# Kernel tuning notes

Hardware: AMD Instinct MI355X
Metric: run time of the kernel (lower is better)

## Reference

```python
import jax, jax.numpy as jnp
import numpy as np

T, D, E, K = 8192, 4096, 64, 8


def setup_inputs() -> dict:
    key = jax.random.key(0)
    k1, k2, k3, k4 = jax.random.split(key, 4)
    x = jax.random.normal(k1, (T, D), dtype=jnp.float32)
    # nn.Linear stores weight as [out_features, in_features]
    Wg = jax.random.normal(k2, (E, D), dtype=jnp.float32) * (1.0 / np.sqrt(D))
    Wc = jax.random.normal(k3, (E, D), dtype=jnp.float32) * (1.0 / np.sqrt(D))
    extra_scale = jnp.zeros((E,), dtype=jnp.float32)  # init zeros as in module
    extra_bias = jax.random.normal(k4, (E,), dtype=jnp.float32) * 0.01
    return {"x": x, "Wg": Wg, "Wc": Wc, "extra_scale": extra_scale,
            "extra_bias": extra_bias, "topk": K}


def reference(x, Wg, Wc, extra_scale, extra_bias, topk):
    # scores = |classifier(x) * silu(gate(x))|, softmax in fp32
    gate = jnp.einsum('td,ed->te', x, Wg)        # [T, E]
    cls = jnp.einsum('td,ed->te', x, Wc)         # [T, E]
    scores = jnp.abs(cls * jax.nn.silu(gate))
    scores = jax.nn.softmax(scores.astype(jnp.float32), axis=-1)
    biased = scores + extra_bias[None, :]        # load-balance bias, used only for selection
    _, indices = jax.lax.top_k(biased, topk)     # [T, K]
    original = 1.0 + scores * extra_scale[None, :]
    weights = jnp.take_along_axis(original, indices, axis=1)  # [T, K]
    return weights.astype(x.dtype), indices
```

## Files before the change

kernel.cpp:

```cpp
#include <hip/hip_runtime.h>
#include <math.h>


#define T_DIM 8192
#define D_DIM 4096
#define E_DIM 64
#define N2    128
#define KTOP  8
#define MB_ROWS 64

#define LDS_H2S 512
#define LDS_PS  1040
#define LDS_RGS (3 * LDS_PS)
#define LDS_BFS (2 * LDS_RGS)

typedef __attribute__((ext_vector_type(8)))  short bfrag8;
typedef __attribute__((ext_vector_type(16))) float f32x16;
typedef __attribute__((ext_vector_type(4)))  float f4;

__device__ __forceinline__ unsigned short f2bf_rne(float f) {
    unsigned int u = __float_as_uint(f);
    unsigned int r = u + 0x7fffu + ((u >> 16) & 1u);
    return (unsigned short)(r >> 16);
}
__device__ __forceinline__ float bf2f(unsigned short h) {
    return __uint_as_float(((unsigned int)h) << 16);
}
__device__ __forceinline__ void split3(float v, unsigned short& h,
                                       unsigned short& m, unsigned short& l) {
    h = f2bf_rne(v);
    const float r1 = v - bf2f(h);
    m = f2bf_rne(r1);
    const float r2 = r1 - bf2f(m);
    l = f2bf_rne(r2);
}

__global__ __launch_bounds__(256)
void router_prep(const float* __restrict__ Wg, const float* __restrict__ Wc,
                 unsigned short* __restrict__ Wpk)
{
    const int t   = blockIdx.x * 256 + threadIdx.x;
    const int col = t >> 9;
    const int ch  = t & 511;
    const int k   = ch << 3;

    const float* src = (col < E_DIM) ? (Wg + (size_t)col * D_DIM)
                                     : (Wc + (size_t)(col - E_DIM) * D_DIM);
    const float4 w0 = ((const float4*)(src + k))[0];
    const float4 w1 = ((const float4*)(src + k))[1];
    const float v[8] = {w0.x, w0.y, w0.z, w0.w, w1.x, w1.y, w1.z, w1.w};

    unsigned short hv[8], mv[8], lv[8];
    #pragma unroll
    for (int j = 0; j < 8; ++j) split3(v[j], hv[j], mv[j], lv[j]);

    const int k32 = k >> 5, h2 = (k >> 4) & 1, lh = (k >> 3) & 1;
    const int n = col >> 5, lane = lh * 32 + (col & 31);
    const size_t base = ((((size_t)k32 * 4 + n) * 3 + 0) * 2 + h2) * 512 + (size_t)lane * 8;
    *(ushort4*)(Wpk + base)          = make_ushort4(hv[0], hv[1], hv[2], hv[3]);
    *(ushort4*)(Wpk + base + 4)      = make_ushort4(hv[4], hv[5], hv[6], hv[7]);
    *(ushort4*)(Wpk + base + 1024)   = make_ushort4(mv[0], mv[1], mv[2], mv[3]);
    *(ushort4*)(Wpk + base + 1028)   = make_ushort4(mv[4], mv[5], mv[6], mv[7]);
    *(ushort4*)(Wpk + base + 2048)   = make_ushort4(lv[0], lv[1], lv[2], lv[3]);
    *(ushort4*)(Wpk + base + 2052)   = make_ushort4(lv[4], lv[5], lv[6], lv[7]);
}

__global__ __launch_bounds__(256, 4)
void router_gemm(const float* __restrict__ x,
                 const unsigned short* __restrict__ Wpk,
                 float* __restrict__ P,
                 int sliceK)
{
    __shared__ unsigned short sF[2 * LDS_BFS];

    const int tid  = threadIdx.x;
    const int lane = tid & 63;
    const int wc   = tid >> 6;
    const int l31  = lane & 31;
    const int lh   = lane >> 5;
    const int mb   = blockIdx.x;
    const int ks   = blockIdx.y;
    const int k0   = ks * sliceK;
    const int NT   = sliceK >> 5;
    const int brow0 = mb * MB_ROWS;

    const int srow = tid >> 3;
    const int kq   = tid & 7;
    const int h2w  = kq >> 2;
    const int lew  = ((kq >> 1) & 1) * 32 + srow;
    const int jw   = (kq & 1) * 4;
    const int wbase = h2w * LDS_H2S + lew * 8 + jw;
    const float* gsrc0 = x + (size_t)(brow0 + srow) * D_DIM + k0 + kq * 4;
    const float* gsrc1 = gsrc0 + (size_t)32 * D_DIM;

    f32x16 acc[2];
    #pragma unroll
    for (int rg = 0; rg < 2; ++rg)
        #pragma unroll
        for (int r = 0; r < 16; ++r) acc[rg][r] = 0.f;

    #define WRITE_HALF(v_, bf_, rg_)                                             \
        {                                                                        \
            ushort4 hv_, mv_, lv_;                                               \
            unsigned short h_, m_, l_;                                           \
            split3((v_).x, h_, m_, l_); hv_.x = h_; mv_.x = m_; lv_.x = l_;      \
            split3((v_).y, h_, m_, l_); hv_.y = h_; mv_.y = m_; lv_.y = l_;      \
            split3((v_).z, h_, m_, l_); hv_.z = h_; mv_.z = m_; lv_.z = l_;      \
            split3((v_).w, h_, m_, l_); hv_.w = h_; mv_.w = m_; lv_.w = l_;      \
            const int o_ = (bf_) * LDS_BFS + (rg_) * LDS_RGS + wbase;            \
            *(ushort4*)&sF[o_]              = hv_;                               \
            *(ushort4*)&sF[o_ + LDS_PS]     = mv_;                               \
            *(ushort4*)&sF[o_ + 2 * LDS_PS] = lv_;                               \
        }

    {
        const f4 v0 = __builtin_nontemporal_load((const f4*)gsrc0);
        const f4 v1 = __builtin_nontemporal_load((const f4*)gsrc1);
        WRITE_HALF(v0, 0, 0);
        WRITE_HALF(v1, 0, 1);
    }
    f4 xa0 = {0,0,0,0}, xa1 = {0,0,0,0};
    f4 xb0 = {0,0,0,0}, xb1 = {0,0,0,0};
    if (NT > 1) {
        xa0 = __builtin_nontemporal_load((const f4*)(gsrc0 + 32));
        xa1 = __builtin_nontemporal_load((const f4*)(gsrc1 + 32));
    }
    asm volatile("s_waitcnt lgkmcnt(0)" ::: "memory");
    __builtin_amdgcn_s_barrier();

    for (int t = 0; t < NT; ++t) {
        const int bf = t & 1;
        const int fbase = bf * LDS_BFS;

        if (t + 2 < NT) {
            xb0 = __builtin_nontemporal_load((const f4*)(gsrc0 + (t + 2) * 32));
            xb1 = __builtin_nontemporal_load((const f4*)(gsrc1 + (t + 2) * 32));
        }

        const size_t k32 = (size_t)((k0 + t * 32) >> 5);
        #pragma unroll
        for (int h2 = 0; h2 < 2; ++h2) {
            const unsigned short* bb =
                Wpk + ((((k32 * 4 + wc) * 3 + 0) * 2 + h2) * 64 + lane) * 8;
            const bfrag8 bh = *(const bfrag8*)(bb);
            const bfrag8 bm = *(const bfrag8*)(bb + 1024);
            const bfrag8 bl = *(const bfrag8*)(bb + 2048);
            #pragma unroll
            for (int rg = 0; rg < 2; ++rg) {
                const int ab = fbase + rg * LDS_RGS + h2 * LDS_H2S + lane * 8;
                const bfrag8 ah = *(const bfrag8*)&sF[ab];
                const bfrag8 am = *(const bfrag8*)&sF[ab + LDS_PS];
                const bfrag8 al = *(const bfrag8*)&sF[ab + 2 * LDS_PS];
                acc[rg] = __builtin_amdgcn_mfma_f32_32x32x16_bf16(ah, bl, acc[rg], 0, 0, 0);
                acc[rg] = __builtin_amdgcn_mfma_f32_32x32x16_bf16(al, bh, acc[rg], 0, 0, 0);
                acc[rg] = __builtin_amdgcn_mfma_f32_32x32x16_bf16(am, bm, acc[rg], 0, 0, 0);
                acc[rg] = __builtin_amdgcn_mfma_f32_32x32x16_bf16(ah, bm, acc[rg], 0, 0, 0);
                acc[rg] = __builtin_amdgcn_mfma_f32_32x32x16_bf16(am, bh, acc[rg], 0, 0, 0);
                acc[rg] = __builtin_amdgcn_mfma_f32_32x32x16_bf16(ah, bh, acc[rg], 0, 0, 0);
            }
        }

        if (t + 1 < NT) {
            WRITE_HALF(xa0, bf ^ 1, 0);
            WRITE_HALF(xa1, bf ^ 1, 1);
        }
        asm volatile("s_waitcnt lgkmcnt(0)" ::: "memory");
        __builtin_amdgcn_s_barrier();
        xa0 = xb0; xa1 = xb1;
    }
    #undef WRITE_HALF

    #pragma unroll
    for (int rg = 0; rg < 2; ++rg) {
        float* Pb = P + ((size_t)ks * T_DIM + brow0 + rg * 32) * N2 + wc * 32 + l31;
        #pragma unroll
        for (int r = 0; r < 16; ++r) {
            const int wrow = (r & 3) + 8 * (r >> 2) + 4 * lh;
            __builtin_nontemporal_store(acc[rg][r], &Pb[(size_t)wrow * N2]);
        }
    }
}

__global__ __launch_bounds__(256)
void router_topk(const float* __restrict__ P,
                 const float* __restrict__ scale,
                 const float* __restrict__ bias,
                 float* __restrict__ out,
                 int ksplit)
{
    const int lane = threadIdx.x & 63;
    const int wid  = threadIdx.x >> 6;
    const int row  = blockIdx.x * 4 + wid;

    float g = 0.f, c = 0.f;
    for (int ks = 0; ks < ksplit; ++ks) {
        const float* p = P + ((size_t)ks * T_DIM + row) * N2;
        g += p[lane];
        c += p[E_DIM + lane];
    }
    const float sg = g / (1.f + expf(-g));
    const float v  = fabsf(c * sg);

    float m = v;
    #pragma unroll
    for (int off = 32; off >= 1; off >>= 1) m = fmaxf(m, __shfl_xor(m, off));
    const float e = expf(v - m);
    float Z = e;
    #pragma unroll
    for (int off = 32; off >= 1; off >>= 1) Z += __shfl_xor(Z, off);
    const float s = e / Z;

    const float sc  = scale[lane];
    float cur = s + bias[lane];

    float myw = 0.f; int myi = 0;
    #pragma unroll
    for (int j = 0; j < KTOP; ++j) {
        float bv = cur; int bi = lane;
        #pragma unroll
        for (int off = 32; off >= 1; off >>= 1) {
            const float ov = __shfl_xor(bv, off);
            const int   oi = __shfl_xor(bi, off);
            if (ov > bv || (ov == bv && oi < bi)) { bv = ov; bi = oi; }
        }
        const float s_bi  = __shfl(s,  bi);
        const float sc_bi = __shfl(sc, bi);
        const float w = 1.f + s_bi * sc_bi;
        if (lane == j)  { myw = w; myi = bi; }
        if (lane == bi) cur = -INFINITY;
    }

    if (lane < KTOP) {
        out[(size_t)row * KTOP + lane] = myw;
        out[(size_t)T_DIM * KTOP + (size_t)row * KTOP + lane] = (float)myi;
    }
}

extern "C" void kernel_launch(void* const* d_in, const int* in_sizes, int n_in,
                              void* d_out, int out_size, void* d_ws, size_t ws_size,
                              hipStream_t stream)
{
    const float* x  = (const float*)d_in[0];
    const float* Wg = (const float*)d_in[1];
    const float* Wc = (const float*)d_in[2];
    const float* sc = (const float*)d_in[3];
    const float* bs = (const float*)d_in[4];
    float* out = (float*)d_out;
    float* P   = (float*)d_ws;

    const size_t PER = (size_t)T_DIM * N2 * sizeof(float);
    const size_t WSP = (size_t)N2 * D_DIM * sizeof(unsigned short);

    int S = 8;
    while (S > 1 && (size_t)S * PER + 3 * WSP > ws_size) S >>= 1;
    const int sliceK = D_DIM / S;

    unsigned short* Wpk = (unsigned short*)((char*)d_ws + (size_t)S * PER);

    router_prep<<<256, 256, 0, stream>>>(Wg, Wc, Wpk);
    router_gemm<<<dim3(T_DIM / MB_ROWS, S), 256, 0, stream>>>(x, Wpk, P, sliceK);
    router_topk<<<T_DIM / 4, 256, 0, stream>>>(P, sc, bs, out, S);
}
```

Measured before the change: 249.0 us.

## Process two K-tiles per barrier with four-slot LDS ring and MFMA priority

Restructures the GEMM main loop to handle two 32-wide K tiles per iteration. It uses a four-slot LDS ring, batches all weight fragment loads for both tiles up front, and prefetches x two tiles ahead. This halves the number of barriers and waitcnts per K slice and raises memory-level parallelism. It also wraps the MFMA block in s_setprio. The cost is double the LDS footprint and more registers, so occupancy is lowered from 4 to 3 blocks per CU. The loop assumes NT is even and silently drops a trailing tile otherwise.

```diff
diff --git a/kernel.cpp b/kernel.cpp
--- a/kernel.cpp
+++ b/kernel.cpp
@@ -12,7 +12,7 @@
 #define LDS_H2S 512
 #define LDS_PS  1040
 #define LDS_RGS (3 * LDS_PS)
-#define LDS_BFS (2 * LDS_RGS)
+#define LDS_TS  (2 * LDS_RGS)
 
 typedef __attribute__((ext_vector_type(8)))  short bfrag8;
 typedef __attribute__((ext_vector_type(16))) float f32x16;
@@ -65,13 +65,13 @@
     *(ushort4*)(Wpk + base + 2052)   = make_ushort4(lv[4], lv[5], lv[6], lv[7]);
 }
 
-__global__ __launch_bounds__(256, 4)
+__global__ __launch_bounds__(256, 3)
 void router_gemm(const float* __restrict__ x,
                  const unsigned short* __restrict__ Wpk,
                  float* __restrict__ P,
                  int sliceK)
 {
-    __shared__ unsigned short sF[2 * LDS_BFS];
+    __shared__ unsigned short sF[4 * LDS_TS];
 
     const int tid  = threadIdx.x;
     const int lane = tid & 63;
@@ -82,6 +82,7 @@
     const int ks   = blockIdx.y;
     const int k0   = ks * sliceK;
     const int NT   = sliceK >> 5;
+    const int NP   = NT >> 1;
     const int brow0 = mb * MB_ROWS;
 
     const int srow = tid >> 3;
@@ -99,7 +100,7 @@
         #pragma unroll
         for (int r = 0; r < 16; ++r) acc[rg][r] = 0.f;
 
-    #define WRITE_HALF(v_, bf_, rg_)                                             \
+    #define WRITE_HALF(v_, slot_, rg_)                                           \
         {                                                                        \
             ushort4 hv_, mv_, lv_;                                               \
             unsigned short h_, m_, l_;                                           \
@@ -107,68 +108,106 @@
             split3((v_).y, h_, m_, l_); hv_.y = h_; mv_.y = m_; lv_.y = l_;      \
             split3((v_).z, h_, m_, l_); hv_.z = h_; mv_.z = m_; lv_.z = l_;      \
             split3((v_).w, h_, m_, l_); hv_.w = h_; mv_.w = m_; lv_.w = l_;      \
-            const int o_ = (bf_) * LDS_BFS + (rg_) * LDS_RGS + wbase;            \
+            const int o_ = (slot_) * LDS_TS + (rg_) * LDS_RGS + wbase;           \
             *(ushort4*)&sF[o_]              = hv_;                               \
             *(ushort4*)&sF[o_ + LDS_PS]     = mv_;                               \
             *(ushort4*)&sF[o_ + 2 * LDS_PS] = lv_;                               \
         }
 
+    #define LOAD_B(SET, t_)                                                      \
+        {                                                                        \
+            const size_t k32_ = (size_t)((k0 + (t_) * 32) >> 5);                 \
+            const unsigned short* bb_ =                                          \
+                Wpk + (((k32_ * 4 + wc) * 3) * 2 * 64 + (size_t)lane) * 8;       \
+            SET##h0 = *(const bfrag8*)(bb_);                                     \
+            SET##m0 = *(const bfrag8*)(bb_ + 1024);                              \
+            SET##l0 = *(const bfrag8*)(bb_ + 2048);                              \
+            SET##h1 = *(const bfrag8*)(bb_ + 512);                               \
+            SET##m1 = *(const bfrag8*)(bb_ + 1536);                              \
+            SET##l1 = *(const bfrag8*)(bb_ + 2560);                              \
+        }
+
+    #define MFMA_STEP(slot_, SET)                                                \
+        {                                                                        \
+            _Pragma("unroll")                                                    \
+            for (int rg = 0; rg < 2; ++rg) {                                     \
+                const int ab = (slot_) * LDS_TS + rg * LDS_RGS + lane * 8;       \
+                const bfrag8 ah0 = *(const bfrag8*)&sF[ab];                      \
+                const bfrag8 am0 = *(const bfrag8*)&sF[ab + LDS_PS];             \
+                const bfrag8 al0 = *(const bfrag8*)&sF[ab + 2 * LDS_PS];         \
+                const bfrag8 ah1 = *(const bfrag8*)&sF[ab + LDS_H2S];            \
+                const bfrag8 am1 = *(const bfrag8*)&sF[ab + LDS_H2S + LDS_PS];   \
+                const bfrag8 al1 = *(const bfrag8*)&sF[ab + LDS_H2S + 2 * LDS_PS]; \
+                acc[rg] = __builtin_amdgcn_mfma_f32_32x32x16_bf16(ah0, SET##l0, acc[rg], 0, 0, 0); \
+                acc[rg] = __builtin_amdgcn_mfma_f32_32x32x16_bf16(al0, SET##h0, acc[rg], 0, 0, 0); \
+                acc[rg] = __builtin_amdgcn_mfma_f32_32x32x16_bf16(am0, SET##m0, acc[rg], 0, 0, 0); \
+                acc[rg] = __builtin_amdgcn_mfma_f32_32x32x16_bf16(ah0, SET##m0, acc[rg], 0, 0, 0); \
+                acc[rg] = __builtin_amdgcn_mfma_f32_32x32x16_bf16(am0, SET##h0, acc[rg], 0, 0, 0); \
+                acc[rg] = __builtin_amdgcn_mfma_f32_32x32x16_bf16(ah0, SET##h0, acc[rg], 0, 0, 0); \
+                acc[rg] = __builtin_amdgcn_mfma_f32_32x32x16_bf16(ah1, SET##l1, acc[rg], 0, 0, 0); \
+                acc[rg] = __builtin_amdgcn_mfma_f32_32x32x16_bf16(al1, SET##h1, acc[rg], 0, 0, 0); \
+                acc[rg] = __builtin_amdgcn_mfma_f32_32x32x16_bf16(am1, SET##m1, acc[rg], 0, 0, 0); \
+                acc[rg] = __builtin_amdgcn_mfma_f32_32x32x16_bf16(ah1, SET##m1, acc[rg], 0, 0, 0); \
+                acc[rg] = __builtin_amdgcn_mfma_f32_32x32x16_bf16(am1, SET##h1, acc[rg], 0, 0, 0); \
+                acc[rg] = __builtin_amdgcn_mfma_f32_32x32x16_bf16(ah1, SET##h1, acc[rg], 0, 0, 0); \
+            }                                                                    \
+        }
+
+    bfrag8 Xh0, Xm0, Xl0, Xh1, Xm1, Xl1;
+    bfrag8 Yh0, Ym0, Yl0, Yh1, Ym1, Yl1;
+
     {
-        const f4 v0 = __builtin_nontemporal_load((const f4*)gsrc0);
-        const f4 v1 = __builtin_nontemporal_load((const f4*)gsrc1);
-        WRITE_HALF(v0, 0, 0);
-        WRITE_HALF(v1, 0, 1);
-    }
-    f4 xa0 = {0,0,0,0}, xa1 = {0,0,0,0};
-    f4 xb0 = {0,0,0,0}, xb1 = {0,0,0,0};
-    if (NT > 1) {
-        xa0 = __builtin_nontemporal_load((const f4*)(gsrc0 + 32));
-        xa1 = __builtin_nontemporal_load((const f4*)(gsrc1 + 32));
+        const f4 t0r0 = __builtin_nontemporal_load((const f4*)(gsrc0));
+        const f4 t0r1 = __builtin_nontemporal_load((const f4*)(gsrc1));
+        const f4 t1r0 = __builtin_nontemporal_load((const f4*)(gsrc0 + 32));
+        const f4 t1r1 = __builtin_nontemporal_load((const f4*)(gsrc1 + 32));
+        WRITE_HALF(t0r0, 0, 0);
+        WRITE_HALF(t0r1, 0, 1);
+        WRITE_HALF(t1r0, 1, 0);
+        WRITE_HALF(t1r1, 1, 1);
+    }
+    f4 xa_a0 = {0,0,0,0}, xa_a1 = {0,0,0,0}, xa_b0 = {0,0,0,0}, xa_b1 = {0,0,0,0};
+    f4 xb_a0, xb_a1, xb_b0, xb_b1;
+    if (NT > 2) {
+        xa_a0 = __builtin_nontemporal_load((const f4*)(gsrc0 + 64));
+        xa_a1 = __builtin_nontemporal_load((const f4*)(gsrc1 + 64));
+        xa_b0 = __builtin_nontemporal_load((const f4*)(gsrc0 + 96));
+        xa_b1 = __builtin_nontemporal_load((const f4*)(gsrc1 + 96));
     }
     asm volatile("s_waitcnt lgkmcnt(0)" ::: "memory");
     __builtin_amdgcn_s_barrier();
 
-    for (int t = 0; t < NT; ++t) {
-        const int bf = t & 1;
-        const int fbase = bf * LDS_BFS;
-
-        if (t + 2 < NT) {
-            xb0 = __builtin_nontemporal_load((const f4*)(gsrc0 + (t + 2) * 32));
-            xb1 = __builtin_nontemporal_load((const f4*)(gsrc1 + (t + 2) * 32));
-        }
-
-        const size_t k32 = (size_t)((k0 + t * 32) >> 5);
-        #pragma unroll
-        for (int h2 = 0; h2 < 2; ++h2) {
-            const unsigned short* bb =
-                Wpk + ((((k32 * 4 + wc) * 3 + 0) * 2 + h2) * 64 + lane) * 8;
-            const bfrag8 bh = *(const bfrag8*)(bb);
-            const bfrag8 bm = *(const bfrag8*)(bb + 1024);
-            const bfrag8 bl = *(const bfrag8*)(bb + 2048);
-            #pragma unroll
-            for (int rg = 0; rg < 2; ++rg) {
-                const int ab = fbase + rg * LDS_RGS + h2 * LDS_H2S + lane * 8;
-                const bfrag8 ah = *(const bfrag8*)&sF[ab];
-                const bfrag8 am = *(const bfrag8*)&sF[ab + LDS_PS];
-                const bfrag8 al = *(const bfrag8*)&sF[ab + 2 * LDS_PS];
-                acc[rg] = __builtin_amdgcn_mfma_f32_32x32x16_bf16(ah, bl, acc[rg], 0, 0, 0);
-                acc[rg] = __builtin_amdgcn_mfma_f32_32x32x16_bf16(al, bh, acc[rg], 0, 0, 0);
-                acc[rg] = __builtin_amdgcn_mfma_f32_32x32x16_bf16(am, bm, acc[rg], 0, 0, 0);
-                acc[rg] = __builtin_amdgcn_mfma_f32_32x32x16_bf16(ah, bm, acc[rg], 0, 0, 0);
-                acc[rg] = __builtin_amdgcn_mfma_f32_32x32x16_bf16(am, bh, acc[rg], 0, 0, 0);
-                acc[rg] = __builtin_amdgcn_mfma_f32_32x32x16_bf16(ah, bh, acc[rg], 0, 0, 0);
-            }
-        }
-
-        if (t + 1 < NT) {
-            WRITE_HALF(xa0, bf ^ 1, 0);
-            WRITE_HALF(xa1, bf ^ 1, 1);
+    for (int p = 0; p < NP; ++p) {
+        const int t0 = 2 * p;
+        const int s0 = t0 & 3, s1 = (t0 + 1) & 3, s2 = (t0 + 2) & 3, s3 = (t0 + 3) & 3;
+
+        LOAD_B(X, t0);
+        LOAD_B(Y, t0 + 1);
+        if (t0 + 4 < NT) {
+            xb_a0 = __builtin_nontemporal_load((const f4*)(gsrc0 + (t0 + 4) * 32));
+            xb_a1 = __builtin_nontemporal_load((const f4*)(gsrc1 + (t0 + 4) * 32));
+            xb_b0 = __builtin_nontemporal_load((const f4*)(gsrc0 + (t0 + 5) * 32));
+            xb_b1 = __builtin_nontemporal_load((const f4*)(gsrc1 + (t0 + 5) * 32));
+        }
+
+        __builtin_amdgcn_s_setprio(1);
+        MFMA_STEP(s0, X);
+        MFMA_STEP(s1, Y);
+        __builtin_amdgcn_s_setprio(0);
+
+        if (t0 + 2 < NT) {
+            WRITE_HALF(xa_a0, s2, 0);
+            WRITE_HALF(xa_a1, s2, 1);
+            WRITE_HALF(xa_b0, s3, 0);
+            WRITE_HALF(xa_b1, s3, 1);
         }
         asm volatile("s_waitcnt lgkmcnt(0)" ::: "memory");
         __builtin_amdgcn_s_barrier();
-        xa0 = xb0; xa1 = xb1;
+        xa_a0 = xb_a0; xa_a1 = xb_a1; xa_b0 = xb_b0; xa_b1 = xb_b1;
     }
     #undef WRITE_HALF
+    #undef LOAD_B
+    #undef MFMA_STEP
 
     #pragma unroll
     for (int rg = 0; rg < 2; ++rg) {
```

New measurement: 255.3 us. +2.5%, slower.
